# Performance work log

Measured on AMD Instinct MI355X. Metric: run time of the kernel, lower is better.

## Reference

```python
import jax, jax.numpy as jnp
import numpy as np

T, S, A, H = 262144, 128, 8, 64
GAMMA, LAM, EPS_CLIP = 0.98, 0.95, 0.1


def setup_inputs() -> dict:
    key = jax.random.key(0)
    ks = jax.random.split(key, 14)
    s = jax.random.normal(ks[0], (T, S), jnp.float32)
    s_prime = jax.random.normal(ks[1], (T, S), jnp.float32)
    r = jax.random.normal(ks[2], (T, 1), jnp.float32)
    done_mask = jnp.ones((T, 1), jnp.float32)
    prob_a = jax.random.uniform(ks[3], (T, 1), jnp.float32) * 0.8 + 0.1
    a = jax.random.randint(ks[4], (T, 1), 0, A, dtype=jnp.int32)
    W1 = jax.random.normal(ks[5], (S, H), jnp.float32) / np.sqrt(S)
    b1 = jnp.zeros((H,), jnp.float32)
    W2 = jax.random.normal(ks[6], (H, H), jnp.float32) / np.sqrt(H)
    b2 = jnp.zeros((H,), jnp.float32)
    Wa = jax.random.normal(ks[7], (H, A), jnp.float32) / np.sqrt(H)
    ba = jnp.zeros((A,), jnp.float32)
    Wc = jax.random.normal(ks[8], (H, 1), jnp.float32) / np.sqrt(H)
    bc = jnp.zeros((1,), jnp.float32)
    return dict(s=s, s_prime=s_prime, r=r, done_mask=done_mask, prob_a=prob_a,
                a=a, W1=W1, b1=b1, W2=W2, b2=b2, Wa=Wa, ba=ba, Wc=Wc, bc=bc)


def _hidden(x, W1, b1, W2, b2):
    h = jax.nn.swish(x @ W1 + b1)
    return jax.nn.swish(h @ W2 + b2)


def reference(s, s_prime, r, done_mask, prob_a, a, W1, b1, W2, b2, Wa, ba, Wc, bc):
    h = _hidden(s, W1, b1, W2, b2)            # [T, H]
    v_s = h @ Wc + bc                         # [T, 1]
    hp = _hidden(s_prime, W1, b1, W2, b2)
    v_sp = hp @ Wc + bc                       # [T, 1]

    td_target = r + GAMMA * v_sp * done_mask  # [T, 1]
    delta = r + GAMMA * v_sp - v_s            # [T, 1] (no done mask, as in source)

    # Faithful replication of the source: transpose to (1, T) and reverse-scan
    # over the (size-1) leading axis, so advantage == delta (stop-gradient).
    delta_t = delta.T                         # [1, T]
    wd_t = jnp.full_like(delta_t, GAMMA * LAM)

    def step(acc, xs):
        wd, td = xs                           # each [T]
        new = td + wd * acc                   # [1, T]
        return new, new

    _, adv = jax.lax.scan(step, jnp.zeros_like(delta_t), (wd_t, delta_t), reverse=True)
    advantage = jax.lax.stop_gradient(adv.reshape(-1, 1))  # [T, 1]

    logits = h @ Wa + ba                      # [T, A]
    pi = jax.nn.softmax(logits, axis=-1)
    pi_a = jnp.take_along_axis(pi, a, axis=1) # [T, 1]

    ratio = jnp.exp(jnp.log(pi_a) - jnp.log(prob_a))
    surr1 = ratio * advantage
    surr2 = jnp.clip(ratio, 1.0 - EPS_CLIP, 1.0 + EPS_CLIP) * advantage

    err = jax.lax.stop_gradient(td_target) - v_s
    abs_err = jnp.abs(err)
    huber = jnp.mean(jnp.where(abs_err <= 1.0, 0.5 * err * err, abs_err - 0.5))

    return -jnp.minimum(surr1, surr2) + huber  # [T, 1]
```

## Files before the change

kernel.cpp:

```cpp
#include <hip/hip_runtime.h>
#include <cstddef>
#include <cstdint>

typedef __attribute__((ext_vector_type(8))) _Float16 f16x8;
typedef __attribute__((ext_vector_type(4))) float f32x4;

constexpr int S = 128;
constexpr int H = 64;
constexpr int A = 8;
constexpr float GAMMA = 0.98f;
constexpr float EPS_CLIP = 0.1f;

__device__ __forceinline__ float swishf(float x) {
    return x * __builtin_amdgcn_rcpf(1.0f + __expf(-x));
}
__device__ __forceinline__ f32x4 mfmaf(f16x8 a, f16x8 b, f32x4 c) {
    return __builtin_amdgcn_mfma_f32_16x16x32_f16(a, b, c, 0, 0, 0);
}

__global__ __launch_bounds__(512, 2) void ppo_fwd(
    const float* __restrict__ s, const float* __restrict__ sp,
    const int* __restrict__ aidx,
    const float* __restrict__ W1, const float* __restrict__ b1,
    const float* __restrict__ W2, const float* __restrict__ b2,
    const float* __restrict__ Wa, const float* __restrict__ ba,
    const float* __restrict__ Wc, const float* __restrict__ bc,
    float* __restrict__ ws_vs, float* __restrict__ ws_pia,
    float* __restrict__ ws_vsp, int nbf)
{
    __shared__ f16x8 sW1[16][64];
    __shared__ f16x8 sW2[8][64];
    __shared__ f16x8 sWh[2][64];
    __shared__ __align__(16) _Float16 hbuf[8][16 * 72];
    __shared__ float hs[8][16 * 11];

    const int tid = threadIdx.x;
    const int pass = (blockIdx.x >= (unsigned)nbf) ? 1 : 0;
    const int rb = blockIdx.x - pass * nbf;
    const float* __restrict__ x = pass ? sp : s;

    for (int idx = tid; idx < 16 * 64; idx += 512) {
        int f = idx >> 6, ll = idx & 63;
        int nt = f >> 2, kk = f & 3;
        int gg = ll >> 4, col = nt * 16 + (ll & 15);
        f16x8 v;
        #pragma unroll
        for (int j = 0; j < 8; ++j)
            v[j] = (_Float16)W1[(kk * 32 + gg * 8 + j) * H + col];
        sW1[f][ll] = v;
    }
    for (int idx = tid; idx < 8 * 64; idx += 512) {
        int f = idx >> 6, ll = idx & 63;
        int nt = f >> 1, kk = f & 1;
        int gg = ll >> 4, col = nt * 16 + (ll & 15);
        f16x8 v;
        #pragma unroll
        for (int j = 0; j < 8; ++j)
            v[j] = (_Float16)W2[(kk * 32 + gg * 8 + j) * H + col];
        sW2[f][ll] = v;
    }
    for (int idx = tid; idx < 2 * 64; idx += 512) {
        int kk = idx >> 6, ll = idx & 63;
        int gg = ll >> 4, q = ll & 15;
        f16x8 v;
        #pragma unroll
        for (int j = 0; j < 8; ++j) {
            int k = kk * 32 + gg * 8 + j;
            v[j] = (_Float16)((q == 0) ? Wc[k] : ((q <= 8) ? Wa[k * A + (q - 1)] : 0.0f));
        }
        sWh[kk][ll] = v;
    }
    __syncthreads();

    const int w = tid >> 6, l = tid & 63, g = l >> 4, n15 = l & 15;
    _Float16* hb = hbuf[w];
    float* hsw = hs[w];

    float b1r[4], b2r[4];
    #pragma unroll
    for (int nt = 0; nt < 4; ++nt) { b1r[nt] = b1[nt * 16 + n15]; b2r[nt] = b2[nt * 16 + n15]; }
    const float bhr = (n15 == 0) ? bc[0] : ((n15 <= 8) ? ba[n15 - 1] : 0.0f);

    for (int mt2 = 0; mt2 < 2; ++mt2) {
        const int t0 = rb * 512 + w * 64 + mt2 * 32;

        f16x8 ax[2][4];
        #pragma unroll
        for (int tile = 0; tile < 2; ++tile) {
            const float* row = x + (size_t)(t0 + tile * 16 + n15) * S + g * 8;
            #pragma unroll
            for (int kk = 0; kk < 4; ++kk) {
                float4 v0 = *reinterpret_cast<const float4*>(row + kk * 32);
                float4 v1 = *reinterpret_cast<const float4*>(row + kk * 32 + 4);
                f16x8 a;
                a[0] = (_Float16)v0.x; a[1] = (_Float16)v0.y;
                a[2] = (_Float16)v0.z; a[3] = (_Float16)v0.w;
                a[4] = (_Float16)v1.x; a[5] = (_Float16)v1.y;
                a[6] = (_Float16)v1.z; a[7] = (_Float16)v1.w;
                ax[tile][kk] = a;
            }
        }
        int act[2] = {0, 0};
        if (pass == 0 && l < 16) {
            act[0] = aidx[t0 + l];
            act[1] = aidx[t0 + 16 + l];
        }

        f32x4 acc[2][4];
        #pragma unroll
        for (int tile = 0; tile < 2; ++tile)
            #pragma unroll
            for (int nt = 0; nt < 4; ++nt)
                acc[tile][nt] = (f32x4){b1r[nt], b1r[nt], b1r[nt], b1r[nt]};
        #pragma unroll
        for (int nt = 0; nt < 4; ++nt)
            #pragma unroll
            for (int kk = 0; kk < 4; ++kk) {
                f16x8 bw = sW1[nt * 4 + kk][l];
                acc[0][nt] = mfmaf(ax[0][kk], bw, acc[0][nt]);
                acc[1][nt] = mfmaf(ax[1][kk], bw, acc[1][nt]);
            }

        f16x8 a2[2][2];
        #pragma unroll
        for (int tile = 0; tile < 2; ++tile) {
            #pragma unroll
            for (int nt = 0; nt < 4; ++nt)
                #pragma unroll
                for (int rj = 0; rj < 4; ++rj)
                    hb[(g * 4 + rj) * 72 + nt * 16 + n15] =
                        (_Float16)swishf(acc[tile][nt][rj]);
            #pragma unroll
            for (int kk = 0; kk < 2; ++kk)
                a2[tile][kk] = *reinterpret_cast<f16x8*>(&hb[n15 * 72 + kk * 32 + g * 8]);
        }

        f32x4 acc2[2][4];
        #pragma unroll
        for (int tile = 0; tile < 2; ++tile)
            #pragma unroll
            for (int nt = 0; nt < 4; ++nt)
                acc2[tile][nt] = (f32x4){b2r[nt], b2r[nt], b2r[nt], b2r[nt]};
        #pragma unroll
        for (int nt = 0; nt < 4; ++nt)
            #pragma unroll
            for (int kk = 0; kk < 2; ++kk) {
                f16x8 bw = sW2[nt * 2 + kk][l];
                acc2[0][nt] = mfmaf(a2[0][kk], bw, acc2[0][nt]);
                acc2[1][nt] = mfmaf(a2[1][kk], bw, acc2[1][nt]);
            }

        f16x8 a3[2][2];
        #pragma unroll
        for (int tile = 0; tile < 2; ++tile) {
            #pragma unroll
            for (int nt = 0; nt < 4; ++nt)
                #pragma unroll
                for (int rj = 0; rj < 4; ++rj)
                    hb[(g * 4 + rj) * 72 + nt * 16 + n15] =
                        (_Float16)swishf(acc2[tile][nt][rj]);
            #pragma unroll
            for (int kk = 0; kk < 2; ++kk)
                a3[tile][kk] = *reinterpret_cast<f16x8*>(&hb[n15 * 72 + kk * 32 + g * 8]);
        }

        f32x4 ah[2] = {(f32x4){bhr, bhr, bhr, bhr}, (f32x4){bhr, bhr, bhr, bhr}};
        #pragma unroll
        for (int kk = 0; kk < 2; ++kk) {
            f16x8 bw = sWh[kk][l];
            ah[0] = mfmaf(a3[0][kk], bw, ah[0]);
            ah[1] = mfmaf(a3[1][kk], bw, ah[1]);
        }

        if (pass == 1) {
            #pragma unroll
            for (int tile = 0; tile < 2; ++tile)
                if (n15 == 0) {
                    #pragma unroll
                    for (int rj = 0; rj < 4; ++rj)
                        ws_vsp[t0 + tile * 16 + g * 4 + rj] = ah[tile][rj];
                }
        } else {
            #pragma unroll
            for (int tile = 0; tile < 2; ++tile) {
                if (n15 <= 8) {
                    #pragma unroll
                    for (int rj = 0; rj < 4; ++rj)
                        hsw[(g * 4 + rj) * 11 + n15] = ah[tile][rj];
                }
                if (l < 16) {
                    float vs = hsw[l * 11 + 0];
                    float lgq[A];
                    float m = -1e30f;
                    #pragma unroll
                    for (int q = 0; q < A; ++q) {
                        lgq[q] = hsw[l * 11 + 1 + q];
                        m = fmaxf(m, lgq[q]);
                    }
                    float den = 0.f, num = 0.f;
                    #pragma unroll
                    for (int q = 0; q < A; ++q) {
                        float e = __expf(lgq[q] - m);
                        den += e;
                        num = (q == act[tile]) ? e : num;
                    }
                    int t = t0 + tile * 16 + l;
                    ws_vs[t]  = vs;
                    ws_pia[t] = num / den;
                }
            }
        }
    }
}

__global__ __launch_bounds__(256) void ppo_epi(
    const float* __restrict__ r, const float* __restrict__ done,
    const float* __restrict__ prob_a,
    const float* __restrict__ ws_vs, const float* __restrict__ ws_pia,
    const float* __restrict__ ws_vsp,
    float* __restrict__ out, float* __restrict__ partial, int Ttot)
{
    __shared__ float sred[256];
    const int tid = threadIdx.x;
    const int t = blockIdx.x * 256 + tid;

    float he = 0.f;
    if (t < Ttot) {
        float vs  = ws_vs[t];
        float vsp = ws_vsp[t];
        float rr  = r[t];
        float dm  = done[t];
        float ratio = ws_pia[t] / prob_a[t];

        float td_target = fmaf(GAMMA * dm, vsp, rr);
        float delta     = rr + GAMMA * vsp - vs;
        float s1 = ratio * delta;
        float rcl = fminf(fmaxf(ratio, 1.0f - EPS_CLIP), 1.0f + EPS_CLIP);
        float s2 = rcl * delta;
        out[t] = -fminf(s1, s2);

        float err = td_target - vs;
        float ae = fabsf(err);
        he = (ae <= 1.0f) ? (0.5f * err * err) : (ae - 0.5f);
    }

    sred[tid] = he;
    __syncthreads();
    #pragma unroll
    for (int off = 128; off > 0; off >>= 1) {
        if (tid < off) sred[tid] += sred[tid + off];
        __syncthreads();
    }
    if (tid == 0) partial[blockIdx.x] = sred[0];
}

__global__ __launch_bounds__(256) void ppo_finish(
    const float* __restrict__ partial, int nparts, float invT,
    float4* __restrict__ out4, int n4)
{
    __shared__ float sred[256];
    const int tid = threadIdx.x;
    float v = 0.f;
    for (int i = tid; i < nparts; i += 256) v += partial[i];
    sred[tid] = v;
    __syncthreads();
    #pragma unroll
    for (int off = 128; off > 0; off >>= 1) {
        if (tid < off) sred[tid] += sred[tid + off];
        __syncthreads();
    }
    const float m = sred[0] * invT;
    const int i = blockIdx.x * 256 + tid;
    if (i < n4) {
        float4 o = out4[i];
        o.x += m; o.y += m; o.z += m; o.w += m;
        out4[i] = o;
    }
}

extern "C" void kernel_launch(void* const* d_in, const int* in_sizes, int n_in,
                              void* d_out, int out_size, void* d_ws, size_t ws_size,
                              hipStream_t stream)
{
    const float* s      = (const float*)d_in[0];
    const float* sp     = (const float*)d_in[1];
    const float* r      = (const float*)d_in[2];
    const float* done   = (const float*)d_in[3];
    const float* prob_a = (const float*)d_in[4];
    const int*   a      = (const int*)d_in[5];
    const float* W1     = (const float*)d_in[6];
    const float* b1     = (const float*)d_in[7];
    const float* W2     = (const float*)d_in[8];
    const float* b2     = (const float*)d_in[9];
    const float* Wa     = (const float*)d_in[10];
    const float* ba     = (const float*)d_in[11];
    const float* Wc     = (const float*)d_in[12];
    const float* bc     = (const float*)d_in[13];

    float* out = (float*)d_out;
    float* ws  = (float*)d_ws;

    const int Ttot = in_sizes[0] / S;
    const int nbf  = Ttot / 512;
    const int nbe  = Ttot / 256;

    float* ws_vs  = ws;
    float* ws_pia = ws + Ttot;
    float* ws_vsp = ws + 2 * (size_t)Ttot;
    float* partial = ws + 3 * (size_t)Ttot;

    ppo_fwd<<<2 * nbf, 512, 0, stream>>>(s, sp, a, W1, b1, W2, b2, Wa, ba, Wc, bc,
                                         ws_vs, ws_pia, ws_vsp, nbf);
    ppo_epi<<<nbe, 256, 0, stream>>>(r, done, prob_a, ws_vs, ws_pia, ws_vsp,
                                     out, partial, Ttot);

    const int n4 = Ttot / 4;
    ppo_finish<<<(n4 + 255) / 256, 256, 0, stream>>>(partial, nbe,
                                                     1.0f / (float)Ttot,
                                                     (float4*)out, n4);
}
```

Before: 62.49 us.

## Merge epilogue and finish kernels via cooperative grid sync

Fuses the epilogue and the mean-broadcast kernels into one cooperative kernel that writes per-block huber partials, does a grid-wide sync, reduces all partials in every block, then writes each output once. This drops one kernel launch and the read-modify-write pass over the output. In exchange every block redundantly reduces 1024 partials, and the grid sync needs all 1024 blocks to be co-resident, which a cooperative launch may reject or serialize.

```diff
diff --git a/kernel.cpp b/kernel.cpp
--- a/kernel.cpp
+++ b/kernel.cpp
@@ -1,6 +1,9 @@
 #include <hip/hip_runtime.h>
+#include <hip/hip_cooperative_groups.h>
 #include <cstddef>
 #include <cstdint>
+
+namespace cg = cooperative_groups;
 
 typedef __attribute__((ext_vector_type(8))) _Float16 f16x8;
 typedef __attribute__((ext_vector_type(4))) float f32x4;
@@ -213,19 +216,21 @@
     }
 }
 
-__global__ __launch_bounds__(256) void ppo_epi(
+__global__ __launch_bounds__(256) void ppo_tail(
     const float* __restrict__ r, const float* __restrict__ done,
     const float* __restrict__ prob_a,
     const float* __restrict__ ws_vs, const float* __restrict__ ws_pia,
     const float* __restrict__ ws_vsp,
-    float* __restrict__ out, float* __restrict__ partial, int Ttot)
+    float* __restrict__ out, float* __restrict__ partial,
+    int Ttot, float invT)
 {
     __shared__ float sred[256];
     const int tid = threadIdx.x;
     const int t = blockIdx.x * 256 + tid;
-
-    float he = 0.f;
-    if (t < Ttot) {
+    const int nparts = gridDim.x;
+
+    float oval = 0.f, he = 0.f;
+    {
         float vs  = ws_vs[t];
         float vsp = ws_vsp[t];
         float rr  = r[t];
@@ -237,7 +242,7 @@
         float s1 = ratio * delta;
         float rcl = fminf(fmaxf(ratio, 1.0f - EPS_CLIP), 1.0f + EPS_CLIP);
         float s2 = rcl * delta;
-        out[t] = -fminf(s1, s2);
+        oval = -fminf(s1, s2);
 
         float err = td_target - vs;
         float ae = fabsf(err);
@@ -252,14 +257,9 @@
         __syncthreads();
     }
     if (tid == 0) partial[blockIdx.x] = sred[0];
-}
-
-__global__ __launch_bounds__(256) void ppo_finish(
-    const float* __restrict__ partial, int nparts, float invT,
-    float4* __restrict__ out4, int n4)
-{
-    __shared__ float sred[256];
-    const int tid = threadIdx.x;
+
+    cg::this_grid().sync();
+
     float v = 0.f;
     for (int i = tid; i < nparts; i += 256) v += partial[i];
     sred[tid] = v;
@@ -269,13 +269,7 @@
         if (tid < off) sred[tid] += sred[tid + off];
         __syncthreads();
     }
-    const float m = sred[0] * invT;
-    const int i = blockIdx.x * 256 + tid;
-    if (i < n4) {
-        float4 o = out4[i];
-        o.x += m; o.y += m; o.z += m; o.w += m;
-        out4[i] = o;
-    }
+    out[t] = oval + sred[0] * invT;
 }
 
 extern "C" void kernel_launch(void* const* d_in, const int* in_sizes, int n_in,
@@ -311,11 +305,11 @@
 
     ppo_fwd<<<2 * nbf, 512, 0, stream>>>(s, sp, a, W1, b1, W2, b2, Wa, ba, Wc, bc,
                                          ws_vs, ws_pia, ws_vsp, nbf);
-    ppo_epi<<<nbe, 256, 0, stream>>>(r, done, prob_a, ws_vs, ws_pia, ws_vsp,
-                                     out, partial, Ttot);
-
-    const int n4 = Ttot / 4;
-    ppo_finish<<<(n4 + 255) / 256, 256, 0, stream>>>(partial, nbe,
-                                                     1.0f / (float)Ttot,
-                                                     (float4*)out, n4);
-}
+
+    float invT = 1.0f / (float)Ttot;
+    void* args[] = {(void*)&r, (void*)&done, (void*)&prob_a,
+                    (void*)&ws_vs, (void*)&ws_pia, (void*)&ws_vsp,
+                    (void*)&out, (void*)&partial, (void*)&Ttot, (void*)&invT};
+    hipLaunchCooperativeKernel(reinterpret_cast<void*>(ppo_tail),
+                               dim3(nbe), dim3(256), args, 0, stream);
+}
```

New measurement: 113.2 us. 1.81x slower.
